# Kernel optimization log

Measured on AMD Instinct MI355X. Metric: run time of the kernel, lower is better.

Reference implementation:

```python
import math
import jax, jax.numpy as jnp
import numpy as np

K = 7  # kernel_size
PAD = 3  # padding (kernel_size//2)


def _base_kernels():
    # 4 oriented anisotropic Gaussian kernels, [4, K, K]
    sigma1, sigma2 = 2.5, 1.0
    ax = jnp.linspace(-(K // 2), K // 2, K)
    xx, yy = jnp.meshgrid(ax, ax, indexing='ij')
    ks = []
    for theta in (0.0, math.pi / 4, math.pi / 2, 3 * math.pi / 4):
        c, s = math.cos(theta), math.sin(theta)
        x_rot = xx * c + yy * s
        y_rot = -xx * s + yy * c
        k = jnp.exp(-(x_rot ** 2 / (2 * sigma1 ** 2) + y_rot ** 2 / (2 * sigma2 ** 2)))
        ks.append(k / k.sum())
    return jnp.stack(ks, axis=0)


def setup_inputs() -> dict:
    key = jax.random.key(0)
    ks = jax.random.split(key, 8)
    B, C, H, W, mid = 2, 256, 256, 256, 16
    x = jax.random.normal(ks[0], (B, C, H, W), dtype=jnp.float32)
    angle_map = jax.random.uniform(ks[1], (B, H, W), dtype=jnp.float32) * math.pi
    reduce_w = jax.random.normal(ks[2], (mid, C), dtype=jnp.float32) * (1.0 / math.sqrt(C))
    expand_w = jax.random.normal(ks[3], (C, mid), dtype=jnp.float32) * (1.0 / math.sqrt(mid))
    w1 = jax.random.normal(ks[4], (8, 2), dtype=jnp.float32) * (1.0 / math.sqrt(2))
    b1 = jnp.zeros((8,), dtype=jnp.float32)
    w2 = jax.random.normal(ks[5], (4, 8), dtype=jnp.float32) * (1.0 / math.sqrt(8))
    b2 = jnp.zeros((4,), dtype=jnp.float32)
    return {"x": x, "angle_map": angle_map, "reduce_w": reduce_w,
            "expand_w": expand_w, "w1": w1, "b1": b1, "w2": w2, "b2": b2}


def reference(x, angle_map, reduce_w, expand_w, w1, b1, w2, b2):
    B, C, H, W = x.shape
    mid = reduce_w.shape[0]
    base = _base_kernels()  # [4,K,K], constant buffer

    # 1x1 reduce conv
    x_low = jnp.einsum('bchw,mc->bmhw', x, reduce_w)  # [B,mid,H,W]

    # per-pixel mixing weights from angle: MLP(2->8->4) + softmax
    angle_feat = jnp.stack([jnp.sin(2 * angle_map), jnp.cos(2 * angle_map)], axis=-1)  # [B,H,W,2]
    h = jax.nn.relu(jnp.einsum('bhwi,oi->bhwo', angle_feat, w1) + b1)
    weights = jax.nn.softmax(jnp.einsum('bhwi,oi->bhwo', h, w2) + b2, axis=-1)  # [B,H,W,4]

    # reflect pad, then cross-correlate each channel with the 4 base kernels.
    # Equivalent to the original unfold+einsum: out = sum_k w_k * (x_low * base_k)
    x_pad = jnp.pad(x_low, ((0, 0), (0, 0), (PAD, PAD), (PAD, PAD)), mode='reflect')
    Hp, Wp = x_pad.shape[-2:]
    y = jax.lax.conv_general_dilated(
        x_pad.reshape(B * mid, 1, Hp, Wp), base[:, None],  # [4,1,K,K]
        window_strides=(1, 1), padding='VALID')  # [B*mid,4,H,W]
    y = y.reshape(B, mid, 4, H, W)

    out_low = jnp.einsum('bmkhw,bhwk->bmhw', y, weights)  # [B,mid,H,W]
    out = jnp.einsum('bmhw,cm->bchw', out_low, expand_w)  # 1x1 expand conv
    return out
```

## Files before the change

### kernel.cpp

```cpp
#include <hip/hip_runtime.h>

#define H_   256
#define W_   256
#define HW_  65536
#define C_   256
#define MID  16
#define B_   2

__global__ __launch_bounds__(256) void k0_prep(const float* __restrict__ rw,
                                               float* __restrict__ base_out,
                                               float* __restrict__ rwt) {
    __shared__ float s_k[4][49];
    __shared__ float s_inv[4];
    int t = threadIdx.x;
    if (t < 196) {
        int k = t / 49, p = t % 49;
        int i = p / 7, j = p % 7;
        float xx = (float)(i - 3), yy = (float)(j - 3);
        const float cs[4] = {1.0f, 0.70710678118654752f, 0.0f, -0.70710678118654752f};
        const float sn[4] = {0.0f, 0.70710678118654752f, 1.0f, 0.70710678118654752f};
        float c = cs[k], s = sn[k];
        float xr = xx * c + yy * s;
        float yr = -xx * s + yy * c;
        float v = expf(-(xr * xr * 0.08f + yr * yr * 0.5f));
        s_k[k][p] = v;
    }
    __syncthreads();
    if (t < 4) {
        float s = 0.f;
        for (int p = 0; p < 49; ++p) s += s_k[t][p];
        s_inv[t] = 1.0f / s;
    }
    __syncthreads();
    if (t < 196) base_out[t] = s_k[t / 49][t % 49] * s_inv[t / 49];
    for (int idx = t; idx < MID * C_; idx += 256) {
        int c = idx >> 4, m = idx & 15;
        rwt[idx] = rw[m * C_ + c];
    }
}

__global__ __launch_bounds__(256) void k1_reduce(const float* __restrict__ x,
                                                 const float* __restrict__ rwt,
                                                 float* __restrict__ xlow) {
    int g = blockIdx.x * 256 + threadIdx.x;
    int p0 = g * 2;
    int b = p0 >> 16;
    int pix = p0 & (HW_ - 1);
    const float2* xp = (const float2*)(x + (size_t)b * C_ * HW_ + pix);
    float2 acc[MID];
#pragma unroll
    for (int m = 0; m < MID; ++m) acc[m] = make_float2(0.f, 0.f);
#pragma unroll 4
    for (int c = 0; c < C_; ++c) {
        float2 v = xp[c * (HW_ / 2)];
#pragma unroll
        for (int m = 0; m < MID; ++m) {
            float w = rwt[c * MID + m];
            acc[m].x = fmaf(w, v.x, acc[m].x);
            acc[m].y = fmaf(w, v.y, acc[m].y);
        }
    }
    float* ob = xlow + (size_t)b * MID * HW_ + pix;
#pragma unroll
    for (int m = 0; m < MID; ++m) {
        *(float2*)(ob + m * HW_) = acc[m];
    }
}

__global__ __launch_bounds__(256) void k2_fused(const float* __restrict__ xlow,
                                                const float* __restrict__ base,
                                                const float* __restrict__ angle,
                                                const float* __restrict__ w1,
                                                const float* __restrict__ b1,
                                                const float* __restrict__ w2,
                                                const float* __restrict__ b2,
                                                const float* __restrict__ ew,
                                                float* __restrict__ out) {
    int bh = blockIdx.x;
    int b = bh >> 8, h = bh & 255;
    int w = threadIdx.x;

    float a2 = 2.0f * angle[(size_t)b * HW_ + h * W_ + w];
    float f0 = __sinf(a2), f1 = __cosf(a2);
    float hb[8];
#pragma unroll
    for (int j = 0; j < 8; ++j) {
        hb[j] = fmaxf(fmaf(w1[j * 2], f0, fmaf(w1[j * 2 + 1], f1, b1[j])), 0.f);
    }
    float lg[4];
#pragma unroll
    for (int k = 0; k < 4; ++k) {
        float s = b2[k];
#pragma unroll
        for (int j = 0; j < 8; ++j) s = fmaf(w2[k * 8 + j], hb[j], s);
        lg[k] = s;
    }
    float mx = fmaxf(fmaxf(lg[0], lg[1]), fmaxf(lg[2], lg[3]));
    float wk[4];
    float ssum = 0.f;
#pragma unroll
    for (int k = 0; k < 4; ++k) { wk[k] = __expf(lg[k] - mx); ssum += wk[k]; }
    float inv = 1.0f / ssum;
#pragma unroll
    for (int k = 0; k < 4; ++k) wk[k] *= inv;

    float acc[MID];
#pragma unroll
    for (int m = 0; m < MID; ++m) acc[m] = 0.f;
    const float* xb = xlow + (size_t)b * MID * HW_;
    int cc[7];
#pragma unroll
    for (int dx = 0; dx < 7; ++dx) {
        int c0 = w + dx - 3;
        cc[dx] = c0 < 0 ? -c0 : (c0 > 255 ? 510 - c0 : c0);
    }
    for (int dy = 0; dy < 7; ++dy) {
        int hy = h + dy - 3;
        hy = hy < 0 ? -hy : (hy > 255 ? 510 - hy : hy);
        float e[7];
#pragma unroll
        for (int dx = 0; dx < 7; ++dx) {
            int tp = dy * 7 + dx;
            e[dx] = fmaf(wk[0], base[tp],
                    fmaf(wk[1], base[49 + tp],
                    fmaf(wk[2], base[98 + tp], wk[3] * base[147 + tp])));
        }
        const float* rowb = xb + hy * W_;
#pragma unroll
        for (int m = 0; m < MID; ++m) {
            const float* row = rowb + (size_t)m * HW_;
            float s = acc[m];
#pragma unroll
            for (int dx = 0; dx < 7; ++dx) s = fmaf(e[dx], row[cc[dx]], s);
            acc[m] = s;
        }
    }

    float* ob = out + (size_t)b * C_ * HW_ + h * W_ + w;
#pragma unroll 4
    for (int c = 0; c < C_; ++c) {
        float s = 0.f;
#pragma unroll
        for (int m = 0; m < MID; ++m) s = fmaf(ew[c * MID + m], acc[m], s);
        __builtin_nontemporal_store(s, ob + (size_t)c * HW_);
    }
}

extern "C" void kernel_launch(void* const* d_in, const int* in_sizes, int n_in,
                              void* d_out, int out_size, void* d_ws, size_t ws_size,
                              hipStream_t stream) {
    const float* x     = (const float*)d_in[0];
    const float* angle = (const float*)d_in[1];
    const float* rw    = (const float*)d_in[2];
    const float* ew    = (const float*)d_in[3];
    const float* w1    = (const float*)d_in[4];
    const float* b1    = (const float*)d_in[5];
    const float* w2    = (const float*)d_in[6];
    const float* b2    = (const float*)d_in[7];
    float* out = (float*)d_out;

    float* wsf  = (float*)d_ws;
    float* base = wsf;
    float* rwt  = wsf + 256;
    float* xlow = wsf + 8192;

    hipLaunchKernelGGL(k0_prep,  dim3(1),   dim3(256), 0, stream, rw, base, rwt);
    hipLaunchKernelGGL(k1_reduce, dim3(256), dim3(256), 0, stream, x, rwt, xlow);
    hipLaunchKernelGGL(k2_fused, dim3(512), dim3(256), 0, stream,
                       xlow, base, angle, w1, b1, w2, b2, ew, out);
}
```

Baseline: 300.3 us.

## Split fused conv/expand into separate kernels with pixel-major intermediate layout

Restructures the pipeline into a reduce kernel, a depthwise-conv kernel and a separate expand kernel. The intermediate x_low is stored pixel-major with 16 channels contiguous, so the conv can read them with float4 loads. The conv splits the mid channels in two and the expand splits output channels into 8 chunks, which raises the block count and parallelism for the write-bound expand. In exchange it adds a round trip through global memory for out_low and one more kernel launch.

```diff
diff --git a/kernel.cpp b/kernel.cpp
--- a/kernel.cpp
+++ b/kernel.cpp
@@ -39,54 +39,55 @@
     }
 }
 
-__global__ __launch_bounds__(256) void k1_reduce(const float* __restrict__ x,
+__global__ __launch_bounds__(256) void kA_reduce(const float* __restrict__ x,
                                                  const float* __restrict__ rwt,
                                                  float* __restrict__ xlow) {
-    int g = blockIdx.x * 256 + threadIdx.x;
-    int p0 = g * 2;
-    int b = p0 >> 16;
-    int pix = p0 & (HW_ - 1);
-    const float2* xp = (const float2*)(x + (size_t)b * C_ * HW_ + pix);
-    float2 acc[MID];
-#pragma unroll
-    for (int m = 0; m < MID; ++m) acc[m] = make_float2(0.f, 0.f);
-#pragma unroll 4
-    for (int c = 0; c < C_; ++c) {
-        float2 v = xp[c * (HW_ / 2)];
-#pragma unroll
-        for (int m = 0; m < MID; ++m) {
-            float w = rwt[c * MID + m];
-            acc[m].x = fmaf(w, v.x, acc[m].x);
-            acc[m].y = fmaf(w, v.y, acc[m].y);
-        }
-    }
-    float* ob = xlow + (size_t)b * MID * HW_ + pix;
-#pragma unroll
-    for (int m = 0; m < MID; ++m) {
-        *(float2*)(ob + m * HW_) = acc[m];
-    }
-}
-
-__global__ __launch_bounds__(256) void k2_fused(const float* __restrict__ xlow,
-                                                const float* __restrict__ base,
-                                                const float* __restrict__ angle,
-                                                const float* __restrict__ w1,
-                                                const float* __restrict__ b1,
-                                                const float* __restrict__ w2,
-                                                const float* __restrict__ b2,
-                                                const float* __restrict__ ew,
-                                                float* __restrict__ out) {
     int bh = blockIdx.x;
     int b = bh >> 8, h = bh & 255;
     int w = threadIdx.x;
+    const float* xp = x + (size_t)b * C_ * HW_ + h * W_ + w;
+    float acc[MID];
+#pragma unroll
+    for (int m = 0; m < MID; ++m) acc[m] = 0.f;
+    for (int cb = 0; cb < C_; cb += 16) {
+        float xv[16];
+#pragma unroll
+        for (int i = 0; i < 16; ++i)
+            xv[i] = __builtin_nontemporal_load(xp + (size_t)(cb + i) * HW_);
+#pragma unroll
+        for (int i = 0; i < 16; ++i) {
+#pragma unroll
+            for (int m = 0; m < MID; ++m)
+                acc[m] = fmaf(rwt[(cb + i) * MID + m], xv[i], acc[m]);
+        }
+    }
+    float4* op = (float4*)(xlow + ((size_t)b * HW_ + h * W_ + w) * MID);
+    op[0] = make_float4(acc[0], acc[1], acc[2], acc[3]);
+    op[1] = make_float4(acc[4], acc[5], acc[6], acc[7]);
+    op[2] = make_float4(acc[8], acc[9], acc[10], acc[11]);
+    op[3] = make_float4(acc[12], acc[13], acc[14], acc[15]);
+}
+
+__global__ __launch_bounds__(256) void kB_conv(const float* __restrict__ xlow,
+                                               const float* __restrict__ base,
+                                               const float* __restrict__ angle,
+                                               const float* __restrict__ w1,
+                                               const float* __restrict__ b1,
+                                               const float* __restrict__ w2,
+                                               const float* __restrict__ b2,
+                                               float* __restrict__ olow) {
+    int bid = blockIdx.x;
+    int mh = bid & 1;
+    int h = (bid >> 1) & 255;
+    int b = bid >> 9;
+    int w = threadIdx.x;
 
     float a2 = 2.0f * angle[(size_t)b * HW_ + h * W_ + w];
     float f0 = __sinf(a2), f1 = __cosf(a2);
     float hb[8];
 #pragma unroll
-    for (int j = 0; j < 8; ++j) {
+    for (int j = 0; j < 8; ++j)
         hb[j] = fmaxf(fmaf(w1[j * 2], f0, fmaf(w1[j * 2 + 1], f1, b1[j])), 0.f);
-    }
     float lg[4];
 #pragma unroll
     for (int k = 0; k < 4; ++k) {
@@ -104,16 +105,16 @@
 #pragma unroll
     for (int k = 0; k < 4; ++k) wk[k] *= inv;
 
-    float acc[MID];
-#pragma unroll
-    for (int m = 0; m < MID; ++m) acc[m] = 0.f;
-    const float* xb = xlow + (size_t)b * MID * HW_;
     int cc[7];
 #pragma unroll
     for (int dx = 0; dx < 7; ++dx) {
         int c0 = w + dx - 3;
         cc[dx] = c0 < 0 ? -c0 : (c0 > 255 ? 510 - c0 : c0);
     }
+    float acc[8];
+#pragma unroll
+    for (int m = 0; m < 8; ++m) acc[m] = 0.f;
+    const float* xb = xlow + (size_t)b * HW_ * MID + mh * 8;
     for (int dy = 0; dy < 7; ++dy) {
         int hy = h + dy - 3;
         hy = hy < 0 ? -hy : (hy > 255 ? 510 - hy : hy);
@@ -125,24 +126,60 @@
                     fmaf(wk[1], base[49 + tp],
                     fmaf(wk[2], base[98 + tp], wk[3] * base[147 + tp])));
         }
-        const float* rowb = xb + hy * W_;
-#pragma unroll
-        for (int m = 0; m < MID; ++m) {
-            const float* row = rowb + (size_t)m * HW_;
-            float s = acc[m];
-#pragma unroll
-            for (int dx = 0; dx < 7; ++dx) s = fmaf(e[dx], row[cc[dx]], s);
-            acc[m] = s;
+        const float* rowb = xb + (size_t)hy * W_ * MID;
+#pragma unroll
+        for (int dx = 0; dx < 7; ++dx) {
+            const float4* p = (const float4*)(rowb + cc[dx] * MID);
+            float4 v0 = p[0];
+            float4 v1 = p[1];
+            float ed = e[dx];
+            acc[0] = fmaf(ed, v0.x, acc[0]);
+            acc[1] = fmaf(ed, v0.y, acc[1]);
+            acc[2] = fmaf(ed, v0.z, acc[2]);
+            acc[3] = fmaf(ed, v0.w, acc[3]);
+            acc[4] = fmaf(ed, v1.x, acc[4]);
+            acc[5] = fmaf(ed, v1.y, acc[5]);
+            acc[6] = fmaf(ed, v1.z, acc[6]);
+            acc[7] = fmaf(ed, v1.w, acc[7]);
         }
     }
-
-    float* ob = out + (size_t)b * C_ * HW_ + h * W_ + w;
-#pragma unroll 4
-    for (int c = 0; c < C_; ++c) {
-        float s = 0.f;
-#pragma unroll
-        for (int m = 0; m < MID; ++m) s = fmaf(ew[c * MID + m], acc[m], s);
-        __builtin_nontemporal_store(s, ob + (size_t)c * HW_);
+    float4* op = (float4*)(olow + ((size_t)b * HW_ + h * W_ + w) * MID + mh * 8);
+    op[0] = make_float4(acc[0], acc[1], acc[2], acc[3]);
+    op[1] = make_float4(acc[4], acc[5], acc[6], acc[7]);
+}
+
+__global__ __launch_bounds__(256) void kC_expand(const float* __restrict__ olow,
+                                                 const float* __restrict__ ew,
+                                                 float* __restrict__ out) {
+    int bid = blockIdx.x;
+    int cch = bid & 7;
+    int h = (bid >> 3) & 255;
+    int b = bid >> 11;
+    int w = threadIdx.x;
+    const float4* ip = (const float4*)(olow + ((size_t)b * HW_ + h * W_ + w) * MID);
+    float4 m0 = ip[0], m1 = ip[1], m2 = ip[2], m3 = ip[3];
+    float* ob = out + ((size_t)b * C_ + cch * 32) * HW_ + h * W_ + w;
+#pragma unroll 8
+    for (int ci = 0; ci < 32; ++ci) {
+        const float* wc = ew + (size_t)(cch * 32 + ci) * MID;
+        float s;
+        s = wc[0] * m0.x;
+        s = fmaf(wc[1], m0.y, s);
+        s = fmaf(wc[2], m0.z, s);
+        s = fmaf(wc[3], m0.w, s);
+        s = fmaf(wc[4], m1.x, s);
+        s = fmaf(wc[5], m1.y, s);
+        s = fmaf(wc[6], m1.z, s);
+        s = fmaf(wc[7], m1.w, s);
+        s = fmaf(wc[8], m2.x, s);
+        s = fmaf(wc[9], m2.y, s);
+        s = fmaf(wc[10], m2.z, s);
+        s = fmaf(wc[11], m2.w, s);
+        s = fmaf(wc[12], m3.x, s);
+        s = fmaf(wc[13], m3.y, s);
+        s = fmaf(wc[14], m3.z, s);
+        s = fmaf(wc[15], m3.w, s);
+        __builtin_nontemporal_store(s, ob + (size_t)ci * HW_);
     }
 }
 
@@ -163,9 +200,11 @@
     float* base = wsf;
     float* rwt  = wsf + 256;
     float* xlow = wsf + 8192;
-
-    hipLaunchKernelGGL(k0_prep,  dim3(1),   dim3(256), 0, stream, rw, base, rwt);
-    hipLaunchKernelGGL(k1_reduce, dim3(256), dim3(256), 0, stream, x, rwt, xlow);
-    hipLaunchKernelGGL(k2_fused, dim3(512), dim3(256), 0, stream,
-                       xlow, base, angle, w1, b1, w2, b2, ew, out);
-}
+    float* olow = wsf + 8192 + B_ * HW_ * MID;
+
+    hipLaunchKernelGGL(k0_prep,   dim3(1),    dim3(256), 0, stream, rw, base, rwt);
+    hipLaunchKernelGGL(kA_reduce, dim3(512),  dim3(256), 0, stream, x, rwt, xlow);
+    hipLaunchKernelGGL(kB_conv,   dim3(1024), dim3(256), 0, stream,
+                       xlow, base, angle, w1, b1, w2, b2, olow);
+    hipLaunchKernelGGL(kC_expand, dim3(4096), dim3(256), 0, stream, olow, ew, out);
+}
```

After: 295.8 us. Within noise of the previous version (-1.5%).

## Restructure reduce kernel: one pixel per thread, batched nontemporal loads, direct weights

Applied to the files above, without the earlier changes.

The reduce kernel now runs one pixel per thread over 512 blocks instead of two pixels per thread over 256 blocks. It loads 32 channels at a time with nontemporal loads to raise memory-level parallelism, and reads reduce weights straight from the original layout, which drops the transpose in the prep kernel. The aim is more wavefronts in flight and more outstanding loads on a bandwidth-bound 134MB read. The cost is more registers from the 32-wide load batch, and weight reads that are strided per channel but warp-uniform.

```diff
diff --git a/kernel.cpp b/kernel.cpp
--- a/kernel.cpp
+++ b/kernel.cpp
@@ -7,9 +7,7 @@
 #define MID  16
 #define B_   2
 
-__global__ __launch_bounds__(256) void k0_prep(const float* __restrict__ rw,
-                                               float* __restrict__ base_out,
-                                               float* __restrict__ rwt) {
+__global__ __launch_bounds__(256) void k0_prep(float* __restrict__ base_out) {
     __shared__ float s_k[4][49];
     __shared__ float s_inv[4];
     int t = threadIdx.x;
@@ -33,49 +31,45 @@
     }
     __syncthreads();
     if (t < 196) base_out[t] = s_k[t / 49][t % 49] * s_inv[t / 49];
-    for (int idx = t; idx < MID * C_; idx += 256) {
-        int c = idx >> 4, m = idx & 15;
-        rwt[idx] = rw[m * C_ + c];
-    }
 }
 
-__global__ __launch_bounds__(256) void k1_reduce(const float* __restrict__ x,
-                                                 const float* __restrict__ rwt,
+__global__ __launch_bounds__(256) void kA_reduce(const float* __restrict__ x,
+                                                 const float* __restrict__ rw,
                                                  float* __restrict__ xlow) {
-    int g = blockIdx.x * 256 + threadIdx.x;
-    int p0 = g * 2;
-    int b = p0 >> 16;
-    int pix = p0 & (HW_ - 1);
-    const float2* xp = (const float2*)(x + (size_t)b * C_ * HW_ + pix);
-    float2 acc[MID];
+    int bh = blockIdx.x;
+    int b = bh >> 8, h = bh & 255;
+    int w = threadIdx.x;
+    const float* xp = x + (size_t)b * C_ * HW_ + h * W_ + w;
+    float acc[MID];
 #pragma unroll
-    for (int m = 0; m < MID; ++m) acc[m] = make_float2(0.f, 0.f);
-#pragma unroll 4
-    for (int c = 0; c < C_; ++c) {
-        float2 v = xp[c * (HW_ / 2)];
+    for (int m = 0; m < MID; ++m) acc[m] = 0.f;
+    for (int cb = 0; cb < C_; cb += 32) {
+        float xv[32];
 #pragma unroll
-        for (int m = 0; m < MID; ++m) {
-            float w = rwt[c * MID + m];
-            acc[m].x = fmaf(w, v.x, acc[m].x);
-            acc[m].y = fmaf(w, v.y, acc[m].y);
+        for (int i = 0; i < 32; ++i)
+            xv[i] = __builtin_nontemporal_load(xp + (size_t)(cb + i) * HW_);
+#pragma unroll
+        for (int i = 0; i < 32; ++i) {
+#pragma unroll
+            for (int m = 0; m < MID; ++m)
+                acc[m] = fmaf(rw[m * C_ + cb + i], xv[i], acc[m]);
         }
     }
-    float* ob = xlow + (size_t)b * MID * HW_ + pix;
+    float* op = xlow + (size_t)b * MID * HW_ + h * W_ + w;
 #pragma unroll
-    for (int m = 0; m < MID; ++m) {
-        *(float2*)(ob + m * HW_) = acc[m];
-    }
+    for (int m = 0; m < MID; ++m) op[(size_t)m * HW_] = acc[m];
 }
 
-__global__ __launch_bounds__(256) void k2_fused(const float* __restrict__ xlow,
-                                                const float* __restrict__ base,
-                                                const float* __restrict__ angle,
-                                                const float* __restrict__ w1,
-                                                const float* __restrict__ b1,
-                                                const float* __restrict__ w2,
-                                                const float* __restrict__ b2,
-                                                const float* __restrict__ ew,
-                                                float* __restrict__ out) {
+__global__ __launch_bounds__(256) void kBC_conv_expand(
+        const float* __restrict__ xlow,
+        const float* __restrict__ base,
+        const float* __restrict__ angle,
+        const float* __restrict__ w1,
+        const float* __restrict__ b1,
+        const float* __restrict__ w2,
+        const float* __restrict__ b2,
+        const float* __restrict__ ew,
+        float* __restrict__ out) {
     int bh = blockIdx.x;
     int b = bh >> 8, h = bh & 255;
     int w = threadIdx.x;
@@ -84,9 +78,8 @@
     float f0 = __sinf(a2), f1 = __cosf(a2);
     float hb[8];
 #pragma unroll
-    for (int j = 0; j < 8; ++j) {
+    for (int j = 0; j < 8; ++j)
         hb[j] = fmaxf(fmaf(w1[j * 2], f0, fmaf(w1[j * 2 + 1], f1, b1[j])), 0.f);
-    }
     float lg[4];
 #pragma unroll
     for (int k = 0; k < 4; ++k) {
@@ -104,16 +97,16 @@
 #pragma unroll
     for (int k = 0; k < 4; ++k) wk[k] *= inv;
 
-    float acc[MID];
-#pragma unroll
-    for (int m = 0; m < MID; ++m) acc[m] = 0.f;
-    const float* xb = xlow + (size_t)b * MID * HW_;
     int cc[7];
 #pragma unroll
     for (int dx = 0; dx < 7; ++dx) {
         int c0 = w + dx - 3;
         cc[dx] = c0 < 0 ? -c0 : (c0 > 255 ? 510 - c0 : c0);
     }
+    float acc[MID];
+#pragma unroll
+    for (int m = 0; m < MID; ++m) acc[m] = 0.f;
+    const float* xb = xlow + (size_t)b * MID * HW_;
     for (int dy = 0; dy < 7; ++dy) {
         int hy = h + dy - 3;
         hy = hy < 0 ? -hy : (hy > 255 ? 510 - hy : hy);
@@ -125,7 +118,7 @@
                     fmaf(wk[1], base[49 + tp],
                     fmaf(wk[2], base[98 + tp], wk[3] * base[147 + tp])));
         }
-        const float* rowb = xb + hy * W_;
+        const float* rowb = xb + (size_t)hy * W_;
 #pragma unroll
         for (int m = 0; m < MID; ++m) {
             const float* row = rowb + (size_t)m * HW_;
@@ -139,9 +132,10 @@
     float* ob = out + (size_t)b * C_ * HW_ + h * W_ + w;
 #pragma unroll 4
     for (int c = 0; c < C_; ++c) {
-        float s = 0.f;
+        const float* wc = ew + (size_t)c * MID;
+        float s = wc[0] * acc[0];
 #pragma unroll
-        for (int m = 0; m < MID; ++m) s = fmaf(ew[c * MID + m], acc[m], s);
+        for (int m = 1; m < MID; ++m) s = fmaf(wc[m], acc[m], s);
         __builtin_nontemporal_store(s, ob + (size_t)c * HW_);
     }
 }
@@ -161,11 +155,10 @@
 
     float* wsf  = (float*)d_ws;
     float* base = wsf;
-    float* rwt  = wsf + 256;
-    float* xlow = wsf + 8192;
+    float* xlow = wsf + 256;
 
-    hipLaunchKernelGGL(k0_prep,  dim3(1),   dim3(256), 0, stream, rw, base, rwt);
-    hipLaunchKernelGGL(k1_reduce, dim3(256), dim3(256), 0, stream, x, rwt, xlow);
-    hipLaunchKernelGGL(k2_fused, dim3(512), dim3(256), 0, stream,
+    hipLaunchKernelGGL(k0_prep,   dim3(1),   dim3(256), 0, stream, base);
+    hipLaunchKernelGGL(kA_reduce, dim3(512), dim3(256), 0, stream, x, rw, xlow);
+    hipLaunchKernelGGL(kBC_conv_expand, dim3(512), dim3(256), 0, stream,
                        xlow, base, angle, w1, b1, w2, b2, ew, out);
 }
```

New measurement: 356.4 us. 18.7% more time.
